# Performance work log

Measured on AMD Instinct MI355X. Metric: run time of the kernel, lower is better.

The kernel has to match this reference:

```python
import jax, jax.numpy as jnp
import numpy as np

VOCAB = 100000
DIM = 128
B = 16384
K = 20


def setup_inputs() -> dict:
    key = jax.random.key(0)
    k1, k2, k3, k4, k5 = jax.random.split(key, 5)
    initrange = 0.5 / DIM
    u_emb = jax.random.uniform(k1, (VOCAB, DIM), jnp.float32, -initrange, initrange)
    # v_embeddings initialized uniform_(-0, 0) == zeros in the original; use small
    # random values instead so gradients/loss are non-degenerate for testing.
    v_emb = jax.random.uniform(k2, (VOCAB, DIM), jnp.float32, -initrange, initrange)
    u_pos = jax.random.randint(k3, (B,), 0, VOCAB)
    v_pos = jax.random.randint(k4, (B,), 0, VOCAB)
    v_neg = jax.random.randint(k5, (B, K), 0, VOCAB)
    return {"u_emb": u_emb, "v_emb": v_emb, "u_pos": u_pos, "v_pos": v_pos,
            "v_neg": v_neg, "batch_size": B}


def reference(u_emb, v_emb, u_pos, v_pos, v_neg, batch_size):
    embed_u = u_emb[u_pos]            # [B, D]
    embed_v = v_emb[v_pos]            # [B, D]
    score = jnp.sum(embed_u * embed_v, axis=1)          # [B]
    log_target = jax.nn.log_sigmoid(score)              # [B]
    neg_embed_v = v_emb[v_neg]        # [B, K, D]
    neg_score = jnp.einsum('bkd,bd->bk', neg_embed_v, embed_u)  # [B, K]
    neg_score = jnp.sum(neg_score, axis=1)               # [B]
    sum_log_sampled = jax.nn.log_sigmoid(-neg_score)     # [B]
    loss = log_target + sum_log_sampled
    return -jnp.sum(loss) / batch_size
```

## Files before the change

kernel.cpp:

```cpp
#include <hip/hip_runtime.h>


constexpr int DIM  = 128;
constexpr int KNEG = 20;
constexpr int WAVES_PER_BLOCK = 4;

__device__ __forceinline__ float log_sigmoid(float x) {
    return fminf(x, 0.0f) - log1pf(__expf(-fabsf(x)));
}

__global__ __launch_bounds__(256) void skipgram_kernel(
    const float* __restrict__ u_emb, const float* __restrict__ v_emb,
    const int* __restrict__ u_pos, const int* __restrict__ v_pos,
    const int* __restrict__ v_neg, float* __restrict__ out,
    int B, float neg_inv_b)
{
    const int wslot = threadIdx.x >> 6;
    const int lane  = threadIdx.x & 63;
    const int gwid  = blockIdx.x * WAVES_PER_BLOCK + wslot;
    const int nwav  = gridDim.x * WAVES_PER_BLOCK;

    float lsum = 0.0f;

    for (int row = gwid; row < B; row += nwav) {
        const int up = u_pos[row];
        const int vp = v_pos[row];
        int idx[KNEG];
        #pragma unroll
        for (int k = 0; k < KNEG; ++k) idx[k] = v_neg[row * KNEG + k];

        const float2 uu = reinterpret_cast<const float2*>(u_emb + (size_t)up * DIM)[lane];
        const float2 vv = reinterpret_cast<const float2*>(v_emb + (size_t)vp * DIM)[lane];

        float2 nv[KNEG];
        #pragma unroll
        for (int k = 0; k < KNEG; ++k)
            nv[k] = reinterpret_cast<const float2*>(v_emb + (size_t)idx[k] * DIM)[lane];

        float pos = fmaf(uu.x, vv.x, uu.y * vv.y);
        float accx = 0.0f, accy = 0.0f;
        #pragma unroll
        for (int k = 0; k < KNEG; ++k) { accx += nv[k].x; accy += nv[k].y; }
        float neg = fmaf(uu.x, accx, uu.y * accy);

        #pragma unroll
        for (int off = 32; off; off >>= 1) {
            pos += __shfl_xor(pos, off);
            neg += __shfl_xor(neg, off);
        }

        lsum += log_sigmoid(pos) + log_sigmoid(-neg);
    }

    __shared__ float wsum[WAVES_PER_BLOCK];
    if (lane == 0) wsum[wslot] = lsum;
    __syncthreads();
    if (threadIdx.x == 0) {
        float s = 0.0f;
        #pragma unroll
        for (int w = 0; w < WAVES_PER_BLOCK; ++w) s += wsum[w];
        atomicAdd(out, s * neg_inv_b);
    }
}

extern "C" void kernel_launch(void* const* d_in, const int* in_sizes, int n_in,
                              void* d_out, int out_size, void* d_ws, size_t ws_size,
                              hipStream_t stream) {
    const float* u_emb = (const float*)d_in[0];
    const float* v_emb = (const float*)d_in[1];
    const int*   u_pos = (const int*)d_in[2];
    const int*   v_pos = (const int*)d_in[3];
    const int*   v_neg = (const int*)d_in[4];
    float* out = (float*)d_out;

    const int B = in_sizes[2];

    hipMemsetAsync(out, 0, sizeof(float), stream);

    const int blocks = 1024;
    skipgram_kernel<<<blocks, WAVES_PER_BLOCK * 64, 0, stream>>>(
        u_emb, v_emb, u_pos, v_pos, v_neg, out, B, -1.0f / (float)B);
}
```

Measured before the change: 40.66 us.

## Process two rows per wave with float4 loads and one row per half-wave

Each 64-lane wave now handles two rows at once: each half-wave of 32 lanes reads a 128-float row with float4 loads instead of float2 across 64 lanes. The grid-stride loop is dropped, and the grid is sized so every wave covers exactly one row pair. This gives wider memory transactions and more rows in flight, which should help a latency-bound gather. The cost is more blocks and more atomics on the output, 2048 instead of 1024, and float4 registers for all 20 negative samples.

```diff
diff --git a/kernel.cpp b/kernel.cpp
--- a/kernel.cpp
+++ b/kernel.cpp
@@ -15,45 +15,52 @@
     const int* __restrict__ v_neg, float* __restrict__ out,
     int B, float neg_inv_b)
 {
+    const int lane  = threadIdx.x & 63;
     const int wslot = threadIdx.x >> 6;
-    const int lane  = threadIdx.x & 63;
-    const int gwid  = blockIdx.x * WAVES_PER_BLOCK + wslot;
-    const int nwav  = gridDim.x * WAVES_PER_BLOCK;
+    const int half  = lane >> 5;
+    const int l32   = lane & 31;
+    const int pair  = blockIdx.x * WAVES_PER_BLOCK + wslot;
+    const int row   = pair * 2 + half;
 
-    float lsum = 0.0f;
+    float contrib = 0.0f;
 
-    for (int row = gwid; row < B; row += nwav) {
+    if (row < B) {
         const int up = u_pos[row];
         const int vp = v_pos[row];
         int idx[KNEG];
         #pragma unroll
         for (int k = 0; k < KNEG; ++k) idx[k] = v_neg[row * KNEG + k];
 
-        const float2 uu = reinterpret_cast<const float2*>(u_emb + (size_t)up * DIM)[lane];
-        const float2 vv = reinterpret_cast<const float2*>(v_emb + (size_t)vp * DIM)[lane];
+        const float4 uu = reinterpret_cast<const float4*>(u_emb + (size_t)up * DIM)[l32];
+        const float4 vv = reinterpret_cast<const float4*>(v_emb + (size_t)vp * DIM)[l32];
 
-        float2 nv[KNEG];
+        float4 nv[KNEG];
         #pragma unroll
         for (int k = 0; k < KNEG; ++k)
-            nv[k] = reinterpret_cast<const float2*>(v_emb + (size_t)idx[k] * DIM)[lane];
+            nv[k] = reinterpret_cast<const float4*>(v_emb + (size_t)idx[k] * DIM)[l32];
 
-        float pos = fmaf(uu.x, vv.x, uu.y * vv.y);
-        float accx = 0.0f, accy = 0.0f;
+        float pos = fmaf(uu.x, vv.x, fmaf(uu.y, vv.y, fmaf(uu.z, vv.z, uu.w * vv.w)));
+        float ax = 0.0f, ay = 0.0f, az = 0.0f, aw = 0.0f;
         #pragma unroll
-        for (int k = 0; k < KNEG; ++k) { accx += nv[k].x; accy += nv[k].y; }
-        float neg = fmaf(uu.x, accx, uu.y * accy);
+        for (int k = 0; k < KNEG; ++k) {
+            ax += nv[k].x; ay += nv[k].y; az += nv[k].z; aw += nv[k].w;
+        }
+        float neg = fmaf(uu.x, ax, fmaf(uu.y, ay, fmaf(uu.z, az, uu.w * aw)));
 
         #pragma unroll
-        for (int off = 32; off; off >>= 1) {
+        for (int off = 16; off; off >>= 1) {
             pos += __shfl_xor(pos, off);
             neg += __shfl_xor(neg, off);
         }
 
-        lsum += log_sigmoid(pos) + log_sigmoid(-neg);
+        float loss = log_sigmoid(pos) + log_sigmoid(-neg);
+        contrib = (l32 == 0) ? loss : 0.0f;
     }
 
+    contrib += __shfl_xor(contrib, 32);
+
     __shared__ float wsum[WAVES_PER_BLOCK];
-    if (lane == 0) wsum[wslot] = lsum;
+    if (lane == 0) wsum[wslot] = contrib;
     __syncthreads();
     if (threadIdx.x == 0) {
         float s = 0.0f;
@@ -77,7 +84,8 @@
 
     hipMemsetAsync(out, 0, sizeof(float), stream);
 
-    const int blocks = 1024;
+    const int pairs  = (B + 1) / 2;
+    const int blocks = (pairs + WAVES_PER_BLOCK - 1) / WAVES_PER_BLOCK;
     skipgram_kernel<<<blocks, WAVES_PER_BLOCK * 64, 0, stream>>>(
         u_emb, v_emb, u_pos, v_pos, v_neg, out, B, -1.0f / (float)B);
 }
```

Result: slower. 47.22 us (+16.1%).

## Split negatives across four waves per row and reduce in second kernel

Applied to the files above, without the earlier changes.

Each batch row is now handled by four waves, and each wave gathers five of the twenty negative embeddings, which multiplies the number of independent gathers in flight. Partial scores go to a workspace buffer. A single-block second kernel then combines them and applies log-sigmoid, which replaces the global atomic and the memset. A fallback one-row-per-wave kernel is kept for when the workspace is too small. The cost is an extra launch, a serial single-block reduction over B rows, and the u row being reloaded by four waves.

```diff
diff --git a/kernel.cpp b/kernel.cpp
--- a/kernel.cpp
+++ b/kernel.cpp
@@ -3,62 +3,133 @@
 
 constexpr int DIM  = 128;
 constexpr int KNEG = 20;
-constexpr int WAVES_PER_BLOCK = 4;
+constexpr int SPLIT = 4;
+constexpr int NPW  = KNEG / SPLIT;
 
 __device__ __forceinline__ float log_sigmoid(float x) {
     return fminf(x, 0.0f) - log1pf(__expf(-fabsf(x)));
 }
 
-__global__ __launch_bounds__(256) void skipgram_kernel(
+__global__ __launch_bounds__(256) void skipgram_stage1(
+    const float* __restrict__ u_emb, const float* __restrict__ v_emb,
+    const int* __restrict__ u_pos, const int* __restrict__ v_pos,
+    const int* __restrict__ v_neg,
+    float* __restrict__ pos_arr, float* __restrict__ negp_arr, int B)
+{
+    const int lane  = threadIdx.x & 63;
+    const int wslot = threadIdx.x >> 6;
+    const int gw    = blockIdx.x * 4 + wslot;
+    const int b     = __builtin_amdgcn_readfirstlane(gw >> 2);
+    const int c     = __builtin_amdgcn_readfirstlane(gw & 3);
+    if (b >= B) return;
+
+    const int up = u_pos[b];
+    const int kb = b * KNEG + c * NPW;
+    int idx[NPW];
+    #pragma unroll
+    for (int j = 0; j < NPW; ++j) idx[j] = v_neg[kb + j];
+
+    const float2 uu = reinterpret_cast<const float2*>(u_emb + (size_t)up * DIM)[lane];
+
+    float2 vv = make_float2(0.0f, 0.0f);
+    if (c == 0) {
+        const int vp = v_pos[b];
+        vv = reinterpret_cast<const float2*>(v_emb + (size_t)vp * DIM)[lane];
+    }
+
+    float2 nv[NPW];
+    #pragma unroll
+    for (int j = 0; j < NPW; ++j)
+        nv[j] = reinterpret_cast<const float2*>(v_emb + (size_t)idx[j] * DIM)[lane];
+
+    float pos = fmaf(uu.x, vv.x, uu.y * vv.y);
+    float ax = 0.0f, ay = 0.0f;
+    #pragma unroll
+    for (int j = 0; j < NPW; ++j) { ax += nv[j].x; ay += nv[j].y; }
+    float negp = fmaf(uu.x, ax, uu.y * ay);
+
+    #pragma unroll
+    for (int off = 32; off; off >>= 1) {
+        pos  += __shfl_xor(pos,  off);
+        negp += __shfl_xor(negp, off);
+    }
+
+    if (lane == 0) {
+        negp_arr[c * B + b] = negp;
+        if (c == 0) pos_arr[b] = pos;
+    }
+}
+
+__global__ __launch_bounds__(1024) void skipgram_stage2(
+    const float* __restrict__ pos_arr, const float* __restrict__ negp_arr,
+    float* __restrict__ out, int B, float neg_inv_b)
+{
+    float acc = 0.0f;
+    for (int r = threadIdx.x; r < B; r += 1024) {
+        float pos = pos_arr[r];
+        float neg = negp_arr[r] + negp_arr[B + r] + negp_arr[2 * B + r] + negp_arr[3 * B + r];
+        acc += log_sigmoid(pos) + log_sigmoid(-neg);
+    }
+
+    #pragma unroll
+    for (int off = 32; off; off >>= 1) acc += __shfl_xor(acc, off);
+
+    __shared__ float wsum[16];
+    const int lane = threadIdx.x & 63;
+    const int w    = threadIdx.x >> 6;
+    if (lane == 0) wsum[w] = acc;
+    __syncthreads();
+    if (threadIdx.x == 0) {
+        float s = 0.0f;
+        #pragma unroll
+        for (int i = 0; i < 16; ++i) s += wsum[i];
+        out[0] = s * neg_inv_b;
+    }
+}
+
+__global__ __launch_bounds__(256) void skipgram_f32_kernel(
     const float* __restrict__ u_emb, const float* __restrict__ v_emb,
     const int* __restrict__ u_pos, const int* __restrict__ v_pos,
     const int* __restrict__ v_neg, float* __restrict__ out,
     int B, float neg_inv_b)
 {
+    const int lane  = threadIdx.x & 63;
     const int wslot = threadIdx.x >> 6;
-    const int lane  = threadIdx.x & 63;
-    const int gwid  = blockIdx.x * WAVES_PER_BLOCK + wslot;
-    const int nwav  = gridDim.x * WAVES_PER_BLOCK;
+    const int row   = blockIdx.x * 4 + wslot;
 
-    float lsum = 0.0f;
-
-    for (int row = gwid; row < B; row += nwav) {
+    float contrib = 0.0f;
+    if (row < B) {
         const int up = u_pos[row];
         const int vp = v_pos[row];
         int idx[KNEG];
         #pragma unroll
         for (int k = 0; k < KNEG; ++k) idx[k] = v_neg[row * KNEG + k];
-
         const float2 uu = reinterpret_cast<const float2*>(u_emb + (size_t)up * DIM)[lane];
         const float2 vv = reinterpret_cast<const float2*>(v_emb + (size_t)vp * DIM)[lane];
-
-        float2 nv[KNEG];
+        float pos = fmaf(uu.x, vv.x, uu.y * vv.y);
+        float ax = 0.0f, ay = 0.0f;
         #pragma unroll
-        for (int k = 0; k < KNEG; ++k)
-            nv[k] = reinterpret_cast<const float2*>(v_emb + (size_t)idx[k] * DIM)[lane];
-
-        float pos = fmaf(uu.x, vv.x, uu.y * vv.y);
-        float accx = 0.0f, accy = 0.0f;
-        #pragma unroll
-        for (int k = 0; k < KNEG; ++k) { accx += nv[k].x; accy += nv[k].y; }
-        float neg = fmaf(uu.x, accx, uu.y * accy);
-
+        for (int k = 0; k < KNEG; ++k) {
+            float2 nv = reinterpret_cast<const float2*>(v_emb + (size_t)idx[k] * DIM)[lane];
+            ax += nv.x; ay += nv.y;
+        }
+        float neg = fmaf(uu.x, ax, uu.y * ay);
         #pragma unroll
         for (int off = 32; off; off >>= 1) {
             pos += __shfl_xor(pos, off);
             neg += __shfl_xor(neg, off);
         }
-
-        lsum += log_sigmoid(pos) + log_sigmoid(-neg);
+        if (lane != 0) { pos = 0.0f; neg = 0.0f; }
+        contrib = (lane == 0) ? (log_sigmoid(pos) + log_sigmoid(-neg)) : 0.0f;
     }
 
-    __shared__ float wsum[WAVES_PER_BLOCK];
-    if (lane == 0) wsum[wslot] = lsum;
+    __shared__ float wsum[4];
+    if (lane == 0) wsum[wslot] = contrib;
     __syncthreads();
     if (threadIdx.x == 0) {
         float s = 0.0f;
         #pragma unroll
-        for (int w = 0; w < WAVES_PER_BLOCK; ++w) s += wsum[w];
+        for (int w = 0; w < 4; ++w) s += wsum[w];
         atomicAdd(out, s * neg_inv_b);
     }
 }
@@ -75,9 +146,21 @@
 
     const int B = in_sizes[2];
 
-    hipMemsetAsync(out, 0, sizeof(float), stream);
+    const size_t needed = (size_t)(1 + SPLIT) * B * sizeof(float);
+    if (ws_size >= needed) {
+        float* pos_arr  = (float*)d_ws;
+        float* negp_arr = pos_arr + B;
 
-    const int blocks = 1024;
-    skipgram_kernel<<<blocks, WAVES_PER_BLOCK * 64, 0, stream>>>(
-        u_emb, v_emb, u_pos, v_pos, v_neg, out, B, -1.0f / (float)B);
+        const int blocks1 = B;
+        skipgram_stage1<<<blocks1, 256, 0, stream>>>(
+            u_emb, v_emb, u_pos, v_pos, v_neg, pos_arr, negp_arr, B);
+
+        skipgram_stage2<<<1, 1024, 0, stream>>>(
+            pos_arr, negp_arr, out, B, -1.0f / (float)B);
+    } else {
+        hipMemsetAsync(out, 0, sizeof(float), stream);
+        const int blocks = (B + 3) / 4;
+        skipgram_f32_kernel<<<blocks, 256, 0, stream>>>(
+            u_emb, v_emb, u_pos, v_pos, v_neg, out, B, -1.0f / (float)B);
+    }
 }
```

Result: slower. 55.50 us (+36.5%).
